# Kernel tuning notes

Measured on AMD Instinct MI355X. Metric: run time of the kernel, lower is better.

The kernel has to match this reference:

```python
import jax, jax.numpy as jnp
import numpy as np

N_NODES = 100000
N_EDGES = 3200000  # avg degree 32
NFEAT = 512
NOUT = 7
DIMS = [NFEAT, 12, 10, 8, 6, 4, NOUT]  # hard-coded hidden widths from __init__


def setup_inputs() -> dict:
    key = jax.random.key(0)
    ks = jax.random.split(key, 4 + 2 * 6)
    inp = {
        "x": jax.random.normal(ks[0], (N_NODES, NFEAT), dtype=jnp.float32),
        "edge_val": jax.random.uniform(ks[1], (N_EDGES,), dtype=jnp.float32) / 32.0,  # ~normalized adj
        "edge_src": jax.random.randint(ks[2], (N_EDGES,), 0, N_NODES),
        "edge_dst": jax.random.randint(ks[3], (N_EDGES,), 0, N_NODES),
    }
    for i in range(6):
        s = 1.0 / np.sqrt(DIMS[i + 1])  # pygcn reset_parameters: U(-1/sqrt(out), 1/sqrt(out))
        inp[f"W{i+1}"] = jax.random.uniform(ks[4 + 2 * i], (DIMS[i], DIMS[i + 1]), jnp.float32, -s, s)
        inp[f"b{i+1}"] = jax.random.uniform(ks[5 + 2 * i], (DIMS[i + 1],), jnp.float32, -s, s)
    return inp


def reference(x, edge_val, W1, b1, W2, b2, W3, b3, W4, b4, W5, b5, W6, b6,
              edge_src, edge_dst):
    n = x.shape[0]

    def gc(h, W, b):
        s = h @ W                                   # [N, out] dense mm
        m = edge_val[:, None] * s[edge_src]         # gather + scale per edge
        agg = jax.ops.segment_sum(m, edge_dst, num_segments=n)  # spmm scatter
        return agg + b

    tanhshrink = lambda v: v - jnp.tanh(v)

    h = gc(x, W1, b1)                # dropout p=0 -> identity
    h = jax.nn.relu(gc(h, W2, b2))   # eval-mode dropout -> identity
    h = tanhshrink(gc(h, W3, b3))
    h = tanhshrink(gc(h, W4, b4))
    h = gc(h, W5, b5)
    return gc(h, W6, b6)
```

## Files before the change

### kernel.cpp

```cpp
#include <hip/hip_runtime.h>
#include <hip/hip_bf16.h>
#include <math.h>
#include <stdint.h>


#define T_EDGES 12800
#define NB_MAX  1600
#define FCAP    2560

__global__ __launch_bounds__(256) void hist_kernel(const int* __restrict__ dst,
                                                   int* __restrict__ ghist, int E, int NB) {
    __shared__ int h[NB_MAX];
    for (int i = threadIdx.x; i < NB; i += 256) h[i] = 0;
    __syncthreads();
    int base = blockIdx.x * T_EDGES;
    int n = min(T_EDGES, E - base);
    for (int i = threadIdx.x; i < n; i += 256)
        atomicAdd(&h[((unsigned)dst[base + i]) >> 6], 1);
    __syncthreads();
    for (int i = threadIdx.x; i < NB; i += 256)
        ghist[(size_t)blockIdx.x * NB + i] = h[i];
}

__global__ __launch_bounds__(256) void scanA_kernel(const int* __restrict__ ghist,
                                                    int* __restrict__ btot, int NT, int NB) {
    __shared__ int red[256];
    int b = blockIdx.x, t = threadIdx.x;
    int s = 0;
    for (int tt = t; tt < NT; tt += 256) s += ghist[(size_t)tt * NB + b];
    red[t] = s;
    __syncthreads();
    for (int off = 128; off > 0; off >>= 1) {
        if (t < off) red[t] += red[t + off];
        __syncthreads();
    }
    if (t == 0) btot[b] = red[0];
}

__global__ __launch_bounds__(256) void scanB_kernel(const int* __restrict__ btot,
                                                    int* __restrict__ bbase,
                                                    int* __restrict__ bucket_ptr, int NB) {
    __shared__ int part[256];
    int t = threadIdx.x;
    int chunk = (NB + 255) / 256;
    int lo = t * chunk, hi = min(lo + chunk, NB);
    int s = 0;
    for (int i = lo; i < hi; i++) s += btot[i];
    part[t] = s;
    __syncthreads();
    for (int off = 1; off < 256; off <<= 1) {
        int x = (t >= off) ? part[t - off] : 0;
        __syncthreads();
        part[t] += x;
        __syncthreads();
    }
    int run = part[t] - s;
    for (int i = lo; i < hi; i++) {
        bbase[i] = run;
        bucket_ptr[i] = run;
        run += btot[i];
    }
    if (t == 255) bucket_ptr[NB] = run;
}

__global__ __launch_bounds__(256) void scanC_kernel(const int* __restrict__ ghist,
                                                    const int* __restrict__ bbase,
                                                    int* __restrict__ goff, int NT, int NB) {
    __shared__ int part[256];
    int b = blockIdx.x, t = threadIdx.x;
    int v = (t < NT) ? ghist[(size_t)t * NB + b] : 0;
    part[t] = v;
    __syncthreads();
    for (int off = 1; off < 256; off <<= 1) {
        int x = (t >= off) ? part[t - off] : 0;
        __syncthreads();
        part[t] += x;
        __syncthreads();
    }
    if (t < NT) goff[(size_t)t * NB + b] = bbase[b] + part[t] - v;
}

__global__ __launch_bounds__(256) void scatter_kernel(const int* __restrict__ src,
                                                      const int* __restrict__ dst,
                                                      const float* __restrict__ val,
                                                      const int* __restrict__ ghist,
                                                      const int* __restrict__ goff,
                                                      int2* __restrict__ edges, int E, int NB) {
    __shared__ unsigned perm[T_EDGES];
    __shared__ int loff[NB_MAX];
    __shared__ int lcur[NB_MAX];
    __shared__ int part[256];
    int tb = blockIdx.x, t = threadIdx.x;
    int base = tb * T_EDGES;
    int n = min(T_EDGES, E - base);

    int chunk = (NB + 255) / 256;
    int lo = t * chunk, hi = min(lo + chunk, NB);
    int s = 0;
    for (int i = lo; i < hi; i++) {
        int c = ghist[(size_t)tb * NB + i];
        loff[i] = c;
        s += c;
    }
    part[t] = s;
    __syncthreads();
    for (int off = 1; off < 256; off <<= 1) {
        int x = (t >= off) ? part[t - off] : 0;
        __syncthreads();
        part[t] += x;
        __syncthreads();
    }
    int run = part[t] - s;
    for (int i = lo; i < hi; i++) {
        int c = loff[i];
        loff[i] = run;
        lcur[i] = run;
        run += c;
    }
    __syncthreads();

    for (int i = t; i < n; i += 256) {
        unsigned b = ((unsigned)dst[base + i]) >> 6;
        int p = atomicAdd(&lcur[b], 1);
        perm[p] = (unsigned)i | (b << 14);
    }
    __syncthreads();

    for (int o = t; o < n; o += 256) {
        unsigned v = perm[o];
        int li = v & 16383;
        int b  = v >> 14;
        int g  = goff[(size_t)tb * NB + b] + (o - loff[b]);
        int d  = dst[base + li];
        edges[g] = make_int2(src[base + li] | ((d & 63) << 17), __float_as_int(val[base + li]));
    }
}

__global__ __launch_bounds__(256) void finalize_kernel(int2* __restrict__ edges,
                                                       const int* __restrict__ bucket_ptr,
                                                       int* __restrict__ row_ptr, int N) {
    __shared__ int2 recs[FCAP];
    __shared__ int2 recs2[FCAP];
    __shared__ int cnt[64], offs[64], cur[64];
    int b = blockIdx.x, t = threadIdx.x;
    int s0 = bucket_ptr[b], s1 = bucket_ptr[b + 1];
    int ne = min(s1 - s0, FCAP);
    if (t < 64) cnt[t] = 0;
    __syncthreads();
    for (int i = t; i < ne; i += 256) {
        int2 r = edges[s0 + i];
        recs[i] = r;
        atomicAdd(&cnt[(r.x >> 17) & 63], 1);
    }
    __syncthreads();
    if (t == 0) {
        int run = 0;
        for (int i = 0; i < 64; i++) { offs[i] = run; run += cnt[i]; }
    }
    __syncthreads();
    if (t < 64) {
        cur[t] = offs[t];
        int idx = (b << 6) + t;
        if (idx <= N) row_ptr[idx] = s0 + offs[t];
    }
    __syncthreads();
    for (int i = t; i < ne; i += 256) {
        int2 r = recs[i];
        int ld = (r.x >> 17) & 63;
        int p = atomicAdd(&cur[ld], 1);
        recs2[p] = make_int2(r.x & 0x1FFFF, r.y);
    }
    __syncthreads();
    for (int i = t; i < ne; i += 256) edges[s0 + i] = recs2[i];
}

__global__ __launch_bounds__(256) void dense1_kernel(const float* __restrict__ x,
                                                     const float* __restrict__ W,
                                                     float* __restrict__ out, int N) {
    __shared__ float xs[256 * 33];
    const int t    = threadIdx.x;
    const int row0 = blockIdx.x * 256;
    const int r    = row0 + t;

    float acc[12];
#pragma unroll
    for (int j = 0; j < 12; j++) acc[j] = 0.f;

    for (int tile = 0; tile < 16; ++tile) {
#pragma unroll
        for (int i = 0; i < 8; i++) {
            int idx4 = t + 256 * i;
            int flat = idx4 * 4;
            int rl   = flat >> 5;
            int c    = flat & 31;
            int rg   = row0 + rl;
            if (rg >= N) rg = N - 1;
            const float4 v = *(const float4*)(x + (size_t)rg * 512 + tile * 32 + c);
            float* p = &xs[rl * 33 + c];
            p[0] = v.x; p[1] = v.y; p[2] = v.z; p[3] = v.w;
        }
        __syncthreads();
#pragma unroll 8
        for (int kk = 0; kk < 32; ++kk) {
            float xv = xs[t * 33 + kk];
            int k = tile * 32 + kk;
#pragma unroll
            for (int j = 0; j < 12; j++) acc[j] += xv * W[k * 12 + j];
        }
        __syncthreads();
    }
    if (r < N) {
#pragma unroll
        for (int j = 0; j < 12; j++) out[(size_t)r * 12 + j] = acc[j];
    }
}

template <int NV, int DIN, int DOUT, int OSTR, int ACT, bool FINAL>
__global__ __launch_bounds__(256) void layer_kernel(const int2* __restrict__ edges,
                                                    const int* __restrict__ row_ptr,
                                                    const float* __restrict__ s,
                                                    const float* __restrict__ bias,
                                                    const float* __restrict__ W,
                                                    float* __restrict__ out, int N) {
    int nidx = blockIdx.x * 256 + threadIdx.x;
    if (nidx >= N) return;
    int e0 = row_ptr[nidx], e1 = row_ptr[nidx + 1];
    float4 acc[NV];
#pragma unroll
    for (int v = 0; v < NV; v++) acc[v] = make_float4(0.f, 0.f, 0.f, 0.f);
    const float4* sv = (const float4*)s;
    for (int e = e0; e < e1; ++e) {
        int2 ev = edges[e];
        float w = __int_as_float(ev.y);
        const float4* srow = sv + (size_t)ev.x * NV;
#pragma unroll
        for (int v = 0; v < NV; v++) {
            float4 xr = srow[v];
            acc[v].x += w * xr.x; acc[v].y += w * xr.y;
            acc[v].z += w * xr.z; acc[v].w += w * xr.w;
        }
    }
    float h[NV * 4];
#pragma unroll
    for (int v = 0; v < NV; v++) {
        h[4 * v + 0] = acc[v].x; h[4 * v + 1] = acc[v].y;
        h[4 * v + 2] = acc[v].z; h[4 * v + 3] = acc[v].w;
    }
#pragma unroll
    for (int k = 0; k < DIN; k++) {
        float z = h[k] + bias[k];
        if (ACT == 1) z = fmaxf(z, 0.f);
        else if (ACT == 2) z = z - tanhf(z);
        h[k] = z;
    }
    if (FINAL) {
#pragma unroll
        for (int k = 0; k < DIN; k++) out[(size_t)nidx * DIN + k] = h[k];
    } else {
        float o[OSTR];
#pragma unroll
        for (int j = 0; j < OSTR; j++) o[j] = 0.f;
#pragma unroll
        for (int j = 0; j < DOUT; j++) {
            float tj = 0.f;
#pragma unroll
            for (int k = 0; k < DIN; k++) tj += h[k] * W[k * DOUT + j];
            o[j] = tj;
        }
        float4* orow = (float4*)(out + (size_t)nidx * OSTR);
#pragma unroll
        for (int v = 0; v < OSTR / 4; v++)
            orow[v] = make_float4(o[4 * v], o[4 * v + 1], o[4 * v + 2], o[4 * v + 3]);
    }
}


static inline size_t align256(size_t x) { return (x + 255) & ~(size_t)255; }

extern "C" void kernel_launch(void* const* d_in, const int* in_sizes, int n_in,
                              void* d_out, int out_size, void* d_ws, size_t ws_size,
                              hipStream_t stream) {
    const float* x        = (const float*)d_in[0];
    const float* edge_val = (const float*)d_in[1];
    const int*   edge_src = (const int*)d_in[2];
    const int*   edge_dst = (const int*)d_in[3];
    const float* W1 = (const float*)d_in[4];   const float* b1 = (const float*)d_in[5];
    const float* W2 = (const float*)d_in[6];   const float* b2 = (const float*)d_in[7];
    const float* W3 = (const float*)d_in[8];   const float* b3 = (const float*)d_in[9];
    const float* W4 = (const float*)d_in[10];  const float* b4 = (const float*)d_in[11];
    const float* W5 = (const float*)d_in[12];  const float* b5 = (const float*)d_in[13];
    const float* W6 = (const float*)d_in[14];  const float* b6 = (const float*)d_in[15];

    const int N = in_sizes[0] / 512;
    const int E = in_sizes[1];
    float* out = (float*)d_out;

    const int NB = (N + 63) >> 6;
    const int NT = (E + T_EDGES - 1) / T_EDGES;
    const int nb = (N + 255) / 256;

    char* w = (char*)d_ws;
    float* A          = (float*)w;  w += align256((size_t)N * 12 * sizeof(float));
    float* B          = (float*)w;  w += align256((size_t)N * 12 * sizeof(float));
    int*   ghist      = (int*)w;    w += align256((size_t)NT * NB * sizeof(int));
    int*   goff       = (int*)w;    w += align256((size_t)NT * NB * sizeof(int));
    int*   btot       = (int*)w;    w += align256((size_t)NB * sizeof(int));
    int*   bbase      = (int*)w;    w += align256((size_t)NB * sizeof(int));
    int*   bucket_ptr = (int*)w;    w += align256((size_t)(NB + 1) * sizeof(int));
    int*   row_ptr    = (int*)w;    w += align256((size_t)(N + 1) * sizeof(int));
    int2*  edges      = (int2*)w;   w += align256((size_t)E * sizeof(int2));

    hist_kernel<<<NT, 256, 0, stream>>>(edge_dst, ghist, E, NB);
    scanA_kernel<<<NB, 256, 0, stream>>>(ghist, btot, NT, NB);
    scanB_kernel<<<1, 256, 0, stream>>>(btot, bbase, bucket_ptr, NB);
    scanC_kernel<<<NB, 256, 0, stream>>>(ghist, bbase, goff, NT, NB);
    scatter_kernel<<<NT, 256, 0, stream>>>(edge_src, edge_dst, edge_val, ghist, goff, edges, E, NB);
    finalize_kernel<<<NB, 256, 0, stream>>>(edges, bucket_ptr, row_ptr, N);

    dense1_kernel<<<nb, 256, 0, stream>>>(x, W1, A, N);

    layer_kernel<3, 12, 10, 12, 0, false><<<nb, 256, 0, stream>>>(edges, row_ptr, A, b1, W2, B, N);
    layer_kernel<3, 10, 8, 8, 1, false><<<nb, 256, 0, stream>>>(edges, row_ptr, B, b2, W3, A, N);
    layer_kernel<2, 8, 6, 8, 2, false><<<nb, 256, 0, stream>>>(edges, row_ptr, A, b3, W4, B, N);
    layer_kernel<2, 6, 4, 4, 2, false><<<nb, 256, 0, stream>>>(edges, row_ptr, B, b4, W5, A, N);
    layer_kernel<1, 4, 7, 8, 0, false><<<nb, 256, 0, stream>>>(edges, row_ptr, A, b5, W6, B, N);
    layer_kernel<2, 7, 7, 8, 0, true><<<nb, 256, 0, stream>>>(edges, row_ptr, B, b6, (const float*)nullptr, out, N);
}
```

Before: 834.3 us.

## Switch layer SpMM to edge-balanced bucket blocks with shared-memory segmented accumulation

Each layer kernel now takes one 64-node bucket per block, loads its edges into LDS, and splits them evenly across threads. Each thread accumulates runs of edges that share a destination and flushes them with shared-memory atomics, then 64 threads apply bias, activation and the next weight matrix. The per-node row_ptr is dropped and the local destination stays packed in the edge record, which removes the dst reload in scatter and the per-node load imbalance of one thread per node. In exchange, only 64 of 256 threads do the epilogue, edges beyond FCAP per bucket are silently truncated, and shared-memory atomics are added.

Result: faster. 746.3 us (-10.6%).

```diff
diff --git a/kernel.cpp b/kernel.cpp
--- a/kernel.cpp
+++ b/kernel.cpp
@@ -120,25 +120,25 @@
     __syncthreads();
 
     for (int i = t; i < n; i += 256) {
-        unsigned b = ((unsigned)dst[base + i]) >> 6;
+        int d = dst[base + i];
+        unsigned b = ((unsigned)d) >> 6;
         int p = atomicAdd(&lcur[b], 1);
-        perm[p] = (unsigned)i | (b << 14);
+        perm[p] = (unsigned)i | (b << 14) | ((unsigned)(d & 63) << 25);
     }
     __syncthreads();
 
     for (int o = t; o < n; o += 256) {
         unsigned v = perm[o];
         int li = v & 16383;
-        int b  = v >> 14;
+        int b  = (v >> 14) & 2047;
+        int ld = v >> 25;
         int g  = goff[(size_t)tb * NB + b] + (o - loff[b]);
-        int d  = dst[base + li];
-        edges[g] = make_int2(src[base + li] | ((d & 63) << 17), __float_as_int(val[base + li]));
+        edges[g] = make_int2(src[base + li] | (ld << 17), __float_as_int(val[base + li]));
     }
 }
 
 __global__ __launch_bounds__(256) void finalize_kernel(int2* __restrict__ edges,
-                                                       const int* __restrict__ bucket_ptr,
-                                                       int* __restrict__ row_ptr, int N) {
+                                                       const int* __restrict__ bucket_ptr) {
     __shared__ int2 recs[FCAP];
     __shared__ int2 recs2[FCAP];
     __shared__ int cnt[64], offs[64], cur[64];
@@ -158,17 +158,13 @@
         for (int i = 0; i < 64; i++) { offs[i] = run; run += cnt[i]; }
     }
     __syncthreads();
-    if (t < 64) {
-        cur[t] = offs[t];
-        int idx = (b << 6) + t;
-        if (idx <= N) row_ptr[idx] = s0 + offs[t];
-    }
+    if (t < 64) cur[t] = offs[t];
     __syncthreads();
     for (int i = t; i < ne; i += 256) {
         int2 r = recs[i];
         int ld = (r.x >> 17) & 63;
         int p = atomicAdd(&cur[ld], 1);
-        recs2[p] = make_int2(r.x & 0x1FFFF, r.y);
+        recs2[p] = r;
     }
     __syncthreads();
     for (int i = t; i < ne; i += 256) edges[s0 + i] = recs2[i];
@@ -217,60 +213,95 @@
 
 template <int NV, int DIN, int DOUT, int OSTR, int ACT, bool FINAL>
 __global__ __launch_bounds__(256) void layer_kernel(const int2* __restrict__ edges,
-                                                    const int* __restrict__ row_ptr,
+                                                    const int* __restrict__ bucket_ptr,
                                                     const float* __restrict__ s,
                                                     const float* __restrict__ bias,
                                                     const float* __restrict__ W,
                                                     float* __restrict__ out, int N) {
-    int nidx = blockIdx.x * 256 + threadIdx.x;
-    if (nidx >= N) return;
-    int e0 = row_ptr[nidx], e1 = row_ptr[nidx + 1];
-    float4 acc[NV];
-#pragma unroll
-    for (int v = 0; v < NV; v++) acc[v] = make_float4(0.f, 0.f, 0.f, 0.f);
-    const float4* sv = (const float4*)s;
-    for (int e = e0; e < e1; ++e) {
-        int2 ev = edges[e];
-        float w = __int_as_float(ev.y);
-        const float4* srow = sv + (size_t)ev.x * NV;
+    constexpr int ASTR = 13;
+    __shared__ int2  ebuf[FCAP];
+    __shared__ float acc[64 * ASTR];
+    const int b = blockIdx.x, t = threadIdx.x;
+    const int s0 = bucket_ptr[b];
+    const int ne = min(bucket_ptr[b + 1] - s0, FCAP);
+
+    for (int i = t; i < 64 * ASTR; i += 256) acc[i] = 0.f;
+    for (int i = t; i < ne; i += 256) ebuf[i] = edges[s0 + i];
+    __syncthreads();
+
+    const int K  = (ne + 255) >> 8;
+    const int i0 = t * K;
+    const int i1 = min(i0 + K, ne);
+    if (i0 < i1) {
+        const float4* sv = (const float4*)s;
+        float4 a[NV];
+#pragma unroll
+        for (int v = 0; v < NV; v++) a[v] = make_float4(0.f, 0.f, 0.f, 0.f);
+        int cd = (ebuf[i0].x >> 17) & 63;
+        for (int i = i0; i < i1; ++i) {
+            int2 ev = ebuf[i];
+            int ld = (ev.x >> 17) & 63;
+            if (ld != cd) {
+#pragma unroll
+                for (int v = 0; v < NV; v++) {
+                    atomicAdd(&acc[cd * ASTR + 4 * v + 0], a[v].x);
+                    atomicAdd(&acc[cd * ASTR + 4 * v + 1], a[v].y);
+                    atomicAdd(&acc[cd * ASTR + 4 * v + 2], a[v].z);
+                    atomicAdd(&acc[cd * ASTR + 4 * v + 3], a[v].w);
+                    a[v] = make_float4(0.f, 0.f, 0.f, 0.f);
+                }
+                cd = ld;
+            }
+            float w = __int_as_float(ev.y);
+            const float4* srow = sv + (size_t)(ev.x & 0x1FFFF) * NV;
+#pragma unroll
+            for (int v = 0; v < NV; v++) {
+                float4 xr = srow[v];
+                a[v].x += w * xr.x; a[v].y += w * xr.y;
+                a[v].z += w * xr.z; a[v].w += w * xr.w;
+            }
+        }
 #pragma unroll
         for (int v = 0; v < NV; v++) {
-            float4 xr = srow[v];
-            acc[v].x += w * xr.x; acc[v].y += w * xr.y;
-            acc[v].z += w * xr.z; acc[v].w += w * xr.w;
-        }
-    }
-    float h[NV * 4];
-#pragma unroll
-    for (int v = 0; v < NV; v++) {
-        h[4 * v + 0] = acc[v].x; h[4 * v + 1] = acc[v].y;
-        h[4 * v + 2] = acc[v].z; h[4 * v + 3] = acc[v].w;
-    }
-#pragma unroll
-    for (int k = 0; k < DIN; k++) {
-        float z = h[k] + bias[k];
-        if (ACT == 1) z = fmaxf(z, 0.f);
-        else if (ACT == 2) z = z - tanhf(z);
-        h[k] = z;
-    }
-    if (FINAL) {
-#pragma unroll
-        for (int k = 0; k < DIN; k++) out[(size_t)nidx * DIN + k] = h[k];
-    } else {
-        float o[OSTR];
-#pragma unroll
-        for (int j = 0; j < OSTR; j++) o[j] = 0.f;
-#pragma unroll
-        for (int j = 0; j < DOUT; j++) {
-            float tj = 0.f;
-#pragma unroll
-            for (int k = 0; k < DIN; k++) tj += h[k] * W[k * DOUT + j];
-            o[j] = tj;
-        }
-        float4* orow = (float4*)(out + (size_t)nidx * OSTR);
-#pragma unroll
-        for (int v = 0; v < OSTR / 4; v++)
-            orow[v] = make_float4(o[4 * v], o[4 * v + 1], o[4 * v + 2], o[4 * v + 3]);
+            atomicAdd(&acc[cd * ASTR + 4 * v + 0], a[v].x);
+            atomicAdd(&acc[cd * ASTR + 4 * v + 1], a[v].y);
+            atomicAdd(&acc[cd * ASTR + 4 * v + 2], a[v].z);
+            atomicAdd(&acc[cd * ASTR + 4 * v + 3], a[v].w);
+        }
+    }
+    __syncthreads();
+
+    if (t < 64) {
+        int node = (b << 6) + t;
+        if (node < N) {
+            float h[DIN];
+#pragma unroll
+            for (int k = 0; k < DIN; k++) {
+                float z = acc[t * ASTR + k] + bias[k];
+                if (ACT == 1) z = fmaxf(z, 0.f);
+                else if (ACT == 2) z = z - tanhf(z);
+                h[k] = z;
+            }
+            if (FINAL) {
+#pragma unroll
+                for (int k = 0; k < DIN; k++) out[(size_t)node * DIN + k] = h[k];
+            } else {
+                float o[OSTR];
+#pragma unroll
+                for (int j = 0; j < OSTR; j++) o[j] = 0.f;
+#pragma unroll
+                for (int j = 0; j < DOUT; j++) {
+                    float tj = 0.f;
+#pragma unroll
+                    for (int k = 0; k < DIN; k++) tj += h[k] * W[k * DOUT + j];
+                    o[j] = tj;
+                }
+                float4* orow = (float4*)(out + (size_t)node * OSTR);
+#pragma unroll
+                for (int v = 0; v < OSTR / 4; v++)
+                    orow[v] = make_float4(o[4 * v], o[4 * v + 1], o[4 * v + 2], o[4 * v + 3]);
+            }
+        }
     }
 }
 
@@ -307,7 +338,6 @@
     int*   btot       = (int*)w;    w += align256((size_t)NB * sizeof(int));
     int*   bbase      = (int*)w;    w += align256((size_t)NB * sizeof(int));
     int*   bucket_ptr = (int*)w;    w += align256((size_t)(NB + 1) * sizeof(int));
-    int*   row_ptr    = (int*)w;    w += align256((size_t)(N + 1) * sizeof(int));
     int2*  edges      = (int2*)w;   w += align256((size_t)E * sizeof(int2));
 
     hist_kernel<<<NT, 256, 0, stream>>>(edge_dst, ghist, E, NB);
@@ -315,14 +345,14 @@
     scanB_kernel<<<1, 256, 0, stream>>>(btot, bbase, bucket_ptr, NB);
     scanC_kernel<<<NB, 256, 0, stream>>>(ghist, bbase, goff, NT, NB);
     scatter_kernel<<<NT, 256, 0, stream>>>(edge_src, edge_dst, edge_val, ghist, goff, edges, E, NB);
-    finalize_kernel<<<NB, 256, 0, stream>>>(edges, bucket_ptr, row_ptr, N);
+    finalize_kernel<<<NB, 256, 0, stream>>>(edges, bucket_ptr);
 
     dense1_kernel<<<nb, 256, 0, stream>>>(x, W1, A, N);
 
-    layer_kernel<3, 12, 10, 12, 0, false><<<nb, 256, 0, stream>>>(edges, row_ptr, A, b1, W2, B, N);
-    layer_kernel<3, 10, 8, 8, 1, false><<<nb, 256, 0, stream>>>(edges, row_ptr, B, b2, W3, A, N);
-    layer_kernel<2, 8, 6, 8, 2, false><<<nb, 256, 0, stream>>>(edges, row_ptr, A, b3, W4, B, N);
-    layer_kernel<2, 6, 4, 4, 2, false><<<nb, 256, 0, stream>>>(edges, row_ptr, B, b4, W5, A, N);
-    layer_kernel<1, 4, 7, 8, 0, false><<<nb, 256, 0, stream>>>(edges, row_ptr, A, b5, W6, B, N);
-    layer_kernel<2, 7, 7, 8, 0, true><<<nb, 256, 0, stream>>>(edges, row_ptr, B, b6, (const float*)nullptr, out, N);
-}
+    layer_kernel<3, 12, 10, 12, 0, false><<<NB, 256, 0, stream>>>(edges, bucket_ptr, A, b1, W2, B, N);
+    layer_kernel<3, 10, 8, 8, 1, false><<<NB, 256, 0, stream>>>(edges, bucket_ptr, B, b2, W3, A, N);
+    layer_kernel<2, 8, 6, 8, 2, false><<<NB, 256, 0, stream>>>(edges, bucket_ptr, A, b3, W4, B, N);
+    layer_kernel<2, 6, 4, 4, 2, false><<<NB, 256, 0, stream>>>(edges, bucket_ptr, B, b4, W5, A, N);
+    layer_kernel<1, 4, 7, 8, 0, false><<<NB, 256, 0, stream>>>(edges, bucket_ptr, A, b5, W6, B, N);
+    layer_kernel<2, 7, 7, 8, 0, true><<<NB, 256, 0, stream>>>(edges, bucket_ptr, B, b6, (const float*)nullptr, out, N);
+}
```
